# Performance work log

Measured on AMD Instinct MI355X. Metric: run time of the kernel, lower is better.

The kernel has to match this reference:

```python
import jax, jax.numpy as jnp
import numpy as np

B, T, E, H = 2, 2048, 1024, 16


def setup_inputs() -> dict:
    key = jax.random.key(0)
    ks = jax.random.split(key, 6)
    s = lambda k, shape: jax.random.normal(k, shape, dtype=jnp.float32) * 0.02
    return {
        "x": jax.random.normal(ks[0], (B, T, E), dtype=jnp.float32),
        "ln1_g": jnp.ones((E,), jnp.float32),
        "ln1_b": jnp.zeros((E,), jnp.float32),
        "attn_w": s(ks[1], (E, 3 * E)),
        "attn_b": jnp.zeros((3 * E,), jnp.float32),
        "proj_w": s(ks[2], (E, E)),
        "proj_b": jnp.zeros((E,), jnp.float32),
        "ln2_g": jnp.ones((E,), jnp.float32),
        "ln2_b": jnp.zeros((E,), jnp.float32),
        "mlp_w1": s(ks[3], (E, 4 * E)),
        "mlp_b1": jnp.zeros((4 * E,), jnp.float32),
        "mlp_w2": s(ks[4], (4 * E, E)),
        "mlp_b2": jnp.zeros((E,), jnp.float32),
        "w_att": jnp.ones((1,), jnp.float32),
        "w_mlp": jnp.ones((1,), jnp.float32),
    }


def _ln(x, g, b, eps=1e-5):
    m = x.mean(-1, keepdims=True)
    v = ((x - m) ** 2).mean(-1, keepdims=True)
    return (x - m) * jax.lax.rsqrt(v + eps) * g + b


def reference(x, ln1_g, ln1_b, attn_w, attn_b, proj_w, proj_b,
              ln2_g, ln2_b, mlp_w1, mlp_b1, mlp_w2, mlp_b2, w_att, w_mlp):
    Bx, Tx, Ex = x.shape
    hd = Ex // H
    # --- self-attention on ln_1(x) ---
    qkv = _ln(x, ln1_g, ln1_b) @ attn_w + attn_b          # [B,T,3E]
    q, k, v = jnp.split(qkv, 3, axis=-1)
    q = q.reshape(Bx, Tx, H, hd)
    k = k.reshape(Bx, Tx, H, hd)
    v = v.reshape(Bx, Tx, H, hd)
    att = jnp.einsum('bthd,bshd->bhts', q, k) * (1.0 / np.sqrt(hd))  # [B,H,T,T]
    causal = jnp.tril(jnp.ones((Tx, Tx), dtype=bool))
    att = jnp.where(causal, att, -jnp.inf)
    att = jax.nn.softmax(att, axis=-1)
    y = jnp.einsum('bhts,bshd->bthd', att, v).reshape(Bx, Tx, Ex)
    y = y @ proj_w + proj_b
    x = x * w_att + y
    # --- MLP on ln_2(x) ---
    h = _ln(x, ln2_g, ln2_b) @ mlp_w1 + mlp_b1
    h = jax.nn.gelu(h, approximate=False)
    x = x * w_mlp + (h @ mlp_w2 + mlp_b2)
    return x
```

## Files before the change

kernel.cpp:

```cpp
#include <hip/hip_runtime.h>
#include <math.h>

typedef __bf16 bf16;
typedef bf16 bf16x8 __attribute__((ext_vector_type(8)));
typedef bf16 bf16x4 __attribute__((ext_vector_type(4)));
typedef float f32x4 __attribute__((ext_vector_type(4)));

#define MFMA(a, b, c) __builtin_amdgcn_mfma_f32_16x16x32_bf16((a), (b), (c), 0, 0, 0)

#define GLOAD_LDS16(gp, lp)                                                        \
  __builtin_amdgcn_global_load_lds((const __attribute__((address_space(1))) void*)(gp), \
                                   (__attribute__((address_space(3))) void*)(lp), 16, 0, 0)

static const size_t E_WT_ATTN = 0;
static const size_t E_WT_PROJ = 3145728;
static const size_t E_WT_MLP1 = 4194304;
static const size_t E_WT_MLP2 = 8388608;
static const size_t E_LN1     = 12582912;
static const size_t E_QKV     = 16777216;
static const size_t E_VT      = 37748736;
static const size_t E_Y       = 41943040;
static const size_t E_LN2     = 46137344;
static const size_t E_H       = 50331648;
static const size_t BYTE_X2    = 134217728;
static const size_t BYTE_OPART = 150994944;
static const size_t BYTE_ML    = 184549376;
static const size_t BYTE_GPART = 185597952;
static const size_t TOTAL_BYTES = 252706816;

__device__ __align__(4096) unsigned char g_buf[TOTAL_BYTES];

__global__ __launch_bounds__(256) void transpose_all(const float* __restrict__ aw,
                                                     const float* __restrict__ pw,
                                                     const float* __restrict__ m1,
                                                     const float* __restrict__ m2,
                                                     bf16* __restrict__ o_a,
                                                     bf16* __restrict__ o_p,
                                                     bf16* __restrict__ o_m1,
                                                     bf16* __restrict__ o_m2) {
  __shared__ float tile[32][33];
  int bid = blockIdx.x;
  const float* in;
  bf16* out;
  int K, N, tix;
  if (bid < 3072) { in = aw; out = o_a; K = 1024; N = 3072; tix = bid; }
  else if (bid < 4096) { in = pw; out = o_p; K = 1024; N = 1024; tix = bid - 3072; }
  else if (bid < 8192) { in = m1; out = o_m1; K = 1024; N = 4096; tix = bid - 4096; }
  else { in = m2; out = o_m2; K = 4096; N = 1024; tix = bid - 8192; }
  int ntx = N >> 5;
  int bx = tix % ntx, by = tix / ntx;
  int tx = threadIdx.x, ty = threadIdx.y;
#pragma unroll
  for (int i = ty; i < 32; i += 8)
    tile[i][tx] = in[(size_t)(by * 32 + i) * N + bx * 32 + tx];
  __syncthreads();
#pragma unroll
  for (int i = ty; i < 32; i += 8)
    out[(size_t)(bx * 32 + i) * K + by * 32 + tx] = (bf16)tile[tx][i];
}

__global__ __launch_bounds__(256) void ln_bf16(const float* __restrict__ x,
                                               const float* __restrict__ g,
                                               const float* __restrict__ b,
                                               bf16* __restrict__ out) {
  int row = blockIdx.x, tid = threadIdx.x;
  const float* xr = x + ((size_t)row << 10);
  float4 v = *(const float4*)(xr + tid * 4);
  float s = v.x + v.y + v.z + v.w;
  float ss = v.x * v.x + v.y * v.y + v.z * v.z + v.w * v.w;
#pragma unroll
  for (int off = 32; off >= 1; off >>= 1) {
    s += __shfl_down(s, off);
    ss += __shfl_down(ss, off);
  }
  __shared__ float sh[8];
  int wid = tid >> 6;
  if ((tid & 63) == 0) { sh[wid] = s; sh[wid + 4] = ss; }
  __syncthreads();
  float ts = sh[0] + sh[1] + sh[2] + sh[3];
  float tss = sh[4] + sh[5] + sh[6] + sh[7];
  float mean = ts * (1.0f / 1024.0f);
  float var = tss * (1.0f / 1024.0f) - mean * mean;
  float inv = rsqrtf(var + 1e-5f);
  float4 gg = *(const float4*)(g + tid * 4);
  float4 bb = *(const float4*)(b + tid * 4);
  bf16x4 o;
  o[0] = (bf16)((v.x - mean) * inv * gg.x + bb.x);
  o[1] = (bf16)((v.y - mean) * inv * gg.y + bb.y);
  o[2] = (bf16)((v.z - mean) * inv * gg.z + bb.z);
  o[3] = (bf16)((v.w - mean) * inv * gg.w + bb.w);
  *(bf16x4*)(out + ((size_t)row << 10) + tid * 4) = o;
}

template <int EPI>
__global__ __launch_bounds__(512, 2) void gemm256(const bf16* __restrict__ A,
                                                  const bf16* __restrict__ Bt,
                                                  const float* __restrict__ bias,
                                                  bf16* __restrict__ outb,
                                                  float* __restrict__ outf,
                                                  int M, int N, int K, int Kseg) {
  __shared__ __align__(16) bf16 As[2][16384];
  __shared__ __align__(16) bf16 Bs[2][16384];
  int tid = threadIdx.x;
  int nwg = gridDim.x * gridDim.y;
  int bid = blockIdx.y * gridDim.x + blockIdx.x;
  int id2 = ((nwg & 7) == 0) ? ((bid & 7) * (nwg >> 3) + (bid >> 3)) : bid;
  int bx = id2 % gridDim.x, by = id2 / gridDim.x;
  int lane = tid & 63, wid = tid >> 6;
  int wr = wid >> 2, wc = wid & 3;
  int g = lane >> 4, lr = lane & 15;
  f32x4 acc[8][4];
#pragma unroll
  for (int m = 0; m < 8; ++m)
#pragma unroll
    for (int n = 0; n < 4; ++n) acc[m][n] = (f32x4){0.f, 0.f, 0.f, 0.f};
  const bf16* Ab = A + (size_t)by * 256 * K;
  const bf16* Bb = Bt + (size_t)bx * 256 * K;
  int rbase = tid >> 3;
  int srccol = (((tid & 7) ^ (rbase & 7)) << 3);
  const bf16* Asrc = Ab + (size_t)rbase * K + srccol;
  const bf16* Bsrc = Bb + (size_t)rbase * K + srccol;
#define G256_STAGE(buf, k0)                                                \
  {                                                                        \
    _Pragma("unroll") for (int q = 0; q < 4; ++q) {                        \
      GLOAD_LDS16(Asrc + (size_t)(q * 64) * K + (k0), &As[buf][tid * 8 + q * 4096]); \
      GLOAD_LDS16(Bsrc + (size_t)(q * 64) * K + (k0), &Bs[buf][tid * 8 + q * 4096]); \
    }                                                                      \
  }
  int kbeg = blockIdx.z * Kseg;
  int NT = Kseg >> 6;
  G256_STAGE(0, kbeg);
  if (NT > 1) {
    G256_STAGE(1, kbeg + 64);
    asm volatile("s_waitcnt vmcnt(8)" ::: "memory");
  } else {
    asm volatile("s_waitcnt vmcnt(0)" ::: "memory");
  }
  __builtin_amdgcn_sched_barrier(0);
  __builtin_amdgcn_s_barrier();
  int c = 0;
  for (int t = 0; t < NT; ++t) {
    bf16x8 a0[8], b0[4], a1[8], b1[4];
#pragma unroll
    for (int m = 0; m < 8; ++m) {
      int row = wr * 128 + m * 16 + lr;
      a0[m] = *(const bf16x8*)&As[c][row * 64 + ((g ^ (row & 7)) << 3)];
      a1[m] = *(const bf16x8*)&As[c][row * 64 + (((4 + g) ^ (row & 7)) << 3)];
    }
#pragma unroll
    for (int n = 0; n < 4; ++n) {
      int row = wc * 64 + n * 16 + lr;
      b0[n] = *(const bf16x8*)&Bs[c][row * 64 + ((g ^ (row & 7)) << 3)];
      b1[n] = *(const bf16x8*)&Bs[c][row * 64 + (((4 + g) ^ (row & 7)) << 3)];
    }
#pragma unroll
    for (int m = 0; m < 8; ++m)
#pragma unroll
      for (int n = 0; n < 4; ++n) acc[m][n] = MFMA(a0[m], b0[n], acc[m][n]);
    asm volatile("s_waitcnt lgkmcnt(0)" ::: "memory");
    __builtin_amdgcn_sched_barrier(0);
    __builtin_amdgcn_s_barrier();
    if (t + 2 < NT) G256_STAGE(c, kbeg + (t + 2) * 64);
#pragma unroll
    for (int m = 0; m < 8; ++m)
#pragma unroll
      for (int n = 0; n < 4; ++n) acc[m][n] = MFMA(a1[m], b1[n], acc[m][n]);
    if (t + 2 < NT) {
      asm volatile("s_waitcnt vmcnt(8)" ::: "memory");
    } else if (t + 1 < NT) {
      asm volatile("s_waitcnt vmcnt(0)" ::: "memory");
    }
    __builtin_amdgcn_sched_barrier(0);
    __builtin_amdgcn_s_barrier();
    c ^= 1;
  }
#undef G256_STAGE
  if (EPI == 3) {
    float* po = outf + (size_t)blockIdx.z * M * N;
#pragma unroll
    for (int m = 0; m < 8; ++m) {
#pragma unroll
      for (int n = 0; n < 4; ++n) {
        int rg0 = by * 256 + wr * 128 + m * 16 + g * 4;
        int cg = bx * 256 + wc * 64 + n * 16 + lr;
#pragma unroll
        for (int j = 0; j < 4; ++j) po[(size_t)(rg0 + j) * N + cg] = acc[m][n][j];
      }
    }
  } else {
#pragma unroll
    for (int m = 0; m < 8; ++m) {
#pragma unroll
      for (int n = 0; n < 4; ++n) {
        int rg0 = by * 256 + wr * 128 + m * 16 + g * 4;
        int cg = bx * 256 + wc * 64 + n * 16 + lr;
        float bv = bias[cg];
#pragma unroll
        for (int j = 0; j < 4; ++j) {
          float v = acc[m][n][j] + bv;
          size_t idx = (size_t)(rg0 + j) * N + cg;
          if (EPI == 0)
            outb[idx] = (bf16)v;
          else {
            float u = 0.7978845608f * (v + 0.044715f * v * v * v);
            float e = exp2f(u * 2.885390082f);
            float th = 1.0f - 2.0f / (e + 1.0f);
            outb[idx] = (bf16)(0.5f * v * (1.0f + th));
          }
        }
      }
    }
  }
}

__global__ __launch_bounds__(256) void gemm_bt3(const bf16* __restrict__ A,
                                                const bf16* __restrict__ Bt,
                                                float* __restrict__ outf,
                                                int M, int N, int K, int Kseg) {
  __shared__ __align__(16) bf16 As[128 * 32];
  __shared__ __align__(16) bf16 Bs[128 * 32];
  int bx = blockIdx.x, by = blockIdx.y;
  int tid = threadIdx.x;
  int lane = tid & 63, wid = tid >> 6;
  int wr = wid >> 1, wc = wid & 1;
  int g = lane >> 4, lr = lane & 15;
  f32x4 acc[4][4];
#pragma unroll
  for (int m = 0; m < 4; ++m)
#pragma unroll
    for (int n = 0; n < 4; ++n) acc[m][n] = (f32x4){0.f, 0.f, 0.f, 0.f};
  const bf16* Ab = A + (size_t)by * 128 * K;
  const bf16* Bb = Bt + (size_t)bx * 128 * K;
  int srow = tid >> 2;
  int sk8 = (tid & 3) * 8;
  const bf16* Ap0 = Ab + (size_t)srow * K + sk8;
  const bf16* Ap1 = Ab + (size_t)(srow + 64) * K + sk8;
  const bf16* Bp0 = Bb + (size_t)srow * K + sk8;
  const bf16* Bp1 = Bb + (size_t)(srow + 64) * K + sk8;
  bf16* lA0 = As + tid * 8;
  bf16* lA1 = As + 2048 + tid * 8;
  bf16* lB0 = Bs + tid * 8;
  bf16* lB1 = Bs + 2048 + tid * 8;
  int kbeg = blockIdx.z * Kseg;
  int kend = kbeg + Kseg;
  for (int k0 = kbeg; k0 < kend; k0 += 32) {
    GLOAD_LDS16(Ap0 + k0, lA0);
    GLOAD_LDS16(Ap1 + k0, lA1);
    GLOAD_LDS16(Bp0 + k0, lB0);
    GLOAD_LDS16(Bp1 + k0, lB1);
    __syncthreads();
    bf16x8 af[4], bfv[4];
#pragma unroll
    for (int m = 0; m < 4; ++m) af[m] = *(const bf16x8*)(As + (wr * 64 + m * 16 + lr) * 32 + g * 8);
#pragma unroll
    for (int n = 0; n < 4; ++n) bfv[n] = *(const bf16x8*)(Bs + (wc * 64 + n * 16 + lr) * 32 + g * 8);
#pragma unroll
    for (int m = 0; m < 4; ++m)
#pragma unroll
      for (int n = 0; n < 4; ++n) acc[m][n] = MFMA(af[m], bfv[n], acc[m][n]);
    __syncthreads();
  }
  float* po = outf + (size_t)blockIdx.z * M * N;
#pragma unroll
  for (int m = 0; m < 4; ++m) {
#pragma unroll
    for (int n = 0; n < 4; ++n) {
      int rg0 = by * 128 + wr * 64 + m * 16 + g * 4;
      int cg = bx * 128 + wc * 64 + n * 16 + lr;
#pragma unroll
      for (int j = 0; j < 4; ++j) po[(size_t)(rg0 + j) * N + cg] = acc[m][n][j];
    }
  }
}

template <int SK>
__global__ __launch_bounds__(256) void reduce_add(const float* __restrict__ part,
                                                  const float* __restrict__ bias,
                                                  const float* __restrict__ res,
                                                  const float* __restrict__ wsc,
                                                  float* __restrict__ out, int MN, int N) {
  size_t i = ((size_t)blockIdx.x * 256 + threadIdx.x) * 4;
  float4 a = *(const float4*)(part + i);
#pragma unroll
  for (int s = 1; s < SK; ++s) {
    float4 b = *(const float4*)(part + (size_t)s * MN + i);
    a.x += b.x; a.y += b.y; a.z += b.z; a.w += b.w;
  }
  int col = (int)(i & (size_t)(N - 1));
  float4 bv = *(const float4*)(bias + col);
  float4 rv = *(const float4*)(res + i);
  float w = wsc[0];
  float4 o;
  o.x = rv.x * w + a.x + bv.x;
  o.y = rv.y * w + a.y + bv.y;
  o.z = rv.z * w + a.z + bv.z;
  o.w = rv.w * w + a.w + bv.w;
  *(float4*)(out + i) = o;
}

__global__ __launch_bounds__(256) void reduce_ln(const float* __restrict__ part,
                                                 const float* __restrict__ bias,
                                                 const float* __restrict__ res,
                                                 const float* __restrict__ wsc,
                                                 const float* __restrict__ lng,
                                                 const float* __restrict__ lnb,
                                                 float* __restrict__ x2out,
                                                 bf16* __restrict__ lnout) {
  int row = blockIdx.x, tid = threadIdx.x;
  size_t i = ((size_t)row << 10) + tid * 4;
  float4 a = *(const float4*)(part + i);
  float4 b2 = *(const float4*)(part + 4194304 + i);
  float4 rv = *(const float4*)(res + i);
  float4 bv = *(const float4*)(bias + tid * 4);
  float w = wsc[0];
  float4 o;
  o.x = rv.x * w + a.x + b2.x + bv.x;
  o.y = rv.y * w + a.y + b2.y + bv.y;
  o.z = rv.z * w + a.z + b2.z + bv.z;
  o.w = rv.w * w + a.w + b2.w + bv.w;
  *(float4*)(x2out + i) = o;
  float s = o.x + o.y + o.z + o.w;
  float ss = o.x * o.x + o.y * o.y + o.z * o.z + o.w * o.w;
#pragma unroll
  for (int off = 32; off >= 1; off >>= 1) {
    s += __shfl_down(s, off);
    ss += __shfl_down(ss, off);
  }
  __shared__ float sh[8];
  int wid = tid >> 6;
  if ((tid & 63) == 0) { sh[wid] = s; sh[wid + 4] = ss; }
  __syncthreads();
  float ts = sh[0] + sh[1] + sh[2] + sh[3];
  float tss = sh[4] + sh[5] + sh[6] + sh[7];
  float mean = ts * (1.0f / 1024.0f);
  float var = tss * (1.0f / 1024.0f) - mean * mean;
  float inv = rsqrtf(var + 1e-5f);
  float4 gg = *(const float4*)(lng + tid * 4);
  float4 bb = *(const float4*)(lnb + tid * 4);
  bf16x4 ov;
  ov[0] = (bf16)((o.x - mean) * inv * gg.x + bb.x);
  ov[1] = (bf16)((o.y - mean) * inv * gg.y + bb.y);
  ov[2] = (bf16)((o.z - mean) * inv * gg.z + bb.z);
  ov[3] = (bf16)((o.w - mean) * inv * gg.w + bb.w);
  *(bf16x4*)(lnout + ((size_t)row << 10) + tid * 4) = ov;
}

__global__ __launch_bounds__(256) void split_v_t(const bf16* __restrict__ qkv,
                                                 bf16* __restrict__ vT) {
  int t0 = blockIdx.x * 32;
  int bh = blockIdx.y;
  int b = bh >> 4, h = bh & 15;
  __shared__ bf16 tile[32][72];
  int tid = threadIdx.x;
  int d = tid & 63, tl0 = tid >> 6;
#pragma unroll
  for (int p = 0; p < 8; ++p) {
    int tl = p * 4 + tl0;
    tile[tl][d] = qkv[((size_t)(b * 2048 + t0 + tl)) * 3072 + 2048 + h * 64 + d];
  }
  __syncthreads();
  int tl = tid & 31, dq = tid >> 5;
#pragma unroll
  for (int p = 0; p < 8; ++p) {
    int dd = p * 8 + dq;
    vT[((size_t)(bh * 64 + dd)) * 2048 + t0 + tl] = tile[tl][dd];
  }
}

__global__ __launch_bounds__(256) void attn_fwd(const bf16* __restrict__ qkv,
                                                const bf16* __restrict__ vT,
                                                float* __restrict__ o_part,
                                                float* __restrict__ ml_part) {
  __shared__ __align__(16) bf16 Ks[2][4096];
  __shared__ __align__(16) bf16 Vs[2][4096];
  __shared__ bf16 P[4][16][72];
  int id = blockIdx.x;
  int bh = id & 31;
  int seg = (id >> 5) & 1;
  int qi = ((id >> 6) + bh) & 31;
  int tid = threadIdx.x, wid = tid >> 6, lane = tid & 63;
  int g = lane >> 4, lr = lane & 15;
  int b = bh >> 4, h = bh & 15;
  int nk = qi + 1;
  int n0 = (nk + 1) >> 1;
  int kt0 = seg ? n0 : 0;
  int kt1 = seg ? nk : n0;
  int qrow = qi * 64 + wid * 16 + lr;
  const bf16* Qr = qkv + ((size_t)(b * 2048 + qrow)) * 3072 + h * 64;
  const float beta = 0.18033688f;
  bf16x8 qf[2];
  qf[0] = *(const bf16x8*)(Qr + g * 8);
  qf[1] = *(const bf16x8*)(Qr + 32 + g * 8);
#pragma unroll
  for (int kk = 0; kk < 2; ++kk)
#pragma unroll
    for (int e = 0; e < 8; ++e) qf[kk][e] = (bf16)((float)qf[kk][e] * beta);
  int r0 = tid >> 3, cs0 = ((tid & 7) ^ (r0 & 7)) << 3;
  int c1i = tid + 256;
  int r1 = c1i >> 3, cs1 = ((c1i & 7) ^ (r1 & 7)) << 3;
  const bf16* sK0 = qkv + ((size_t)(b * 2048 + r0)) * 3072 + 1024 + h * 64 + cs0;
  const bf16* sK1 = qkv + ((size_t)(b * 2048 + r1)) * 3072 + 1024 + h * 64 + cs1;
  const bf16* sV0 = vT + (size_t)bh * 131072 + (size_t)r0 * 2048 + cs0;
  const bf16* sV1 = vT + (size_t)bh * 131072 + (size_t)r1 * 2048 + cs1;
  bf16* dK0 = &Ks[0][0] + tid * 8;
  bf16* dK1 = &Ks[0][0] + 2048 + tid * 8;
  bf16* dV0 = &Vs[0][0] + tid * 8;
  bf16* dV1 = &Vs[0][0] + 2048 + tid * 8;
#define ATTN_STAGE(bufsel, ktv)                          \
  {                                                      \
    size_t kadv = (size_t)(ktv) * (64 * 3072);           \
    size_t vadv = (size_t)(ktv) * 64;                    \
    int bo = (bufsel) * 4096;                            \
    GLOAD_LDS16(sK0 + kadv, dK0 + bo);                   \
    GLOAD_LDS16(sK1 + kadv, dK1 + bo);                   \
    GLOAD_LDS16(sV0 + vadv, dV0 + bo);                   \
    GLOAD_LDS16(sV1 + vadv, dV1 + bo);                   \
  }
  f32x4 o[4];
#pragma unroll
  for (int n = 0; n < 4; ++n) o[n] = (f32x4){0.f, 0.f, 0.f, 0.f};
  float m = -3e38f, l = 0.f;
  if (kt0 < kt1) ATTN_STAGE(0, kt0);
  __syncthreads();
  int sw = lr & 7;
  int sb = (lane & 48) | (g << 2);
  for (int kt = kt0; kt < kt1; ++kt) {
    int cur = (kt - kt0) & 1;
    if (kt + 1 < kt1) ATTN_STAGE(cur ^ 1, kt + 1);
    const bf16* Kb = &Ks[cur][0];
    const bf16* Vb = &Vs[cur][0];
    f32x4 s[4];
#pragma unroll
    for (int n = 0; n < 4; ++n) s[n] = (f32x4){0.f, 0.f, 0.f, 0.f};
#pragma unroll
    for (int kk = 0; kk < 2; ++kk) {
#pragma unroll
      for (int n = 0; n < 4; ++n) {
        bf16x8 kf = *(const bf16x8*)(Kb + ((n * 16 + lr) << 6) + ((((kk << 2) + g) ^ sw) << 3));
        s[n] = MFMA(kf, qf[kk], s[n]);
      }
    }
    if (kt == qi) {
      int kc0 = kt * 64 + g * 4;
#pragma unroll
      for (int n = 0; n < 4; ++n)
#pragma unroll
        for (int j = 0; j < 4; ++j)
          if ((kc0 + n * 16 + j) > qrow) s[n][j] = -3e38f;
    }
    float mx = s[0][0];
#pragma unroll
    for (int n = 0; n < 4; ++n)
#pragma unroll
      for (int j = 0; j < 4; ++j) mx = fmaxf(mx, s[n][j]);
    mx = fmaxf(mx, __shfl_xor(mx, 16));
    mx = fmaxf(mx, __shfl_xor(mx, 32));
    bool defer = __all(mx <= m + 11.5416f);
    float mn = m, al = 0.f;
    if (!defer) {
      mn = fmaxf(m, mx);
      al = exp2f(m - mn);
      m = mn;
    }
    float rs = 0.f;
    bf16x4 pw[4];
#pragma unroll
    for (int n = 0; n < 4; ++n)
#pragma unroll
      for (int j = 0; j < 4; ++j) {
        float p = exp2f(s[n][j] - mn);
        rs += p;
        pw[n][j] = (bf16)p;
      }
    rs += __shfl_xor(rs, 16);
    rs += __shfl_xor(rs, 32);
    if (defer) {
      l += rs;
    } else {
      l = l * al + rs;
      float alj[4];
#pragma unroll
      for (int j = 0; j < 4; ++j) alj[j] = __shfl(al, sb + j);
#pragma unroll
      for (int n = 0; n < 4; ++n)
#pragma unroll
        for (int j = 0; j < 4; ++j) o[n][j] *= alj[j];
    }
#pragma unroll
    for (int n = 0; n < 4; ++n) *(bf16x4*)&P[wid][lr][n * 16 + g * 4] = pw[n];
#pragma unroll
    for (int kk = 0; kk < 2; ++kk) {
      bf16x8 pf = *(const bf16x8*)&P[wid][lr][kk * 32 + g * 8];
#pragma unroll
      for (int n = 0; n < 4; ++n) {
        bf16x8 vf = *(const bf16x8*)(Vb + ((n * 16 + lr) << 6) + ((((kk << 2) + g) ^ sw) << 3));
        o[n] = MFMA(pf, vf, o[n]);
      }
    }
    __syncthreads();
  }
  float* ob = o_part + (size_t)id * 4096;
#pragma unroll
  for (int n = 0; n < 4; ++n)
#pragma unroll
    for (int j = 0; j < 4; ++j)
      ob[(size_t)(wid * 16 + g * 4 + j) * 64 + n * 16 + lr] = o[n][j];
  if (lane < 16) {
    ml_part[(size_t)id * 128 + (wid * 16 + lane) * 2] = m;
    ml_part[(size_t)id * 128 + (wid * 16 + lane) * 2 + 1] = l;
  }
#undef ATTN_STAGE
}

__global__ __launch_bounds__(256) void attn_combine(const float* __restrict__ o_part,
                                                    const float* __restrict__ ml_part,
                                                    bf16* __restrict__ y) {
  int c = blockIdx.x;
  int bh = c & 31, qi = c >> 5;
  int b = bh >> 4, h = bh & 15;
  int qraw = (qi - bh) & 31;
  size_t id0 = (size_t)bh + ((size_t)qraw << 6);
  size_t id1 = id0 + 32;
  int t = threadIdx.x;
  int r = t >> 2, cq = (t & 3) << 4;
  float m1 = ml_part[id0 * 128 + r * 2], l1 = ml_part[id0 * 128 + r * 2 + 1];
  float m2 = ml_part[id1 * 128 + r * 2], l2 = ml_part[id1 * 128 + r * 2 + 1];
  float mm = fmaxf(m1, m2);
  float w1 = exp2f(m1 - mm), w2 = exp2f(m2 - mm);
  float inv = 1.0f / (l1 * w1 + l2 * w2);
  const float* p1 = o_part + id0 * 4096 + r * 64 + cq;
  const float* p2 = o_part + id1 * 4096 + r * 64 + cq;
  bf16* yp = y + ((size_t)(b * 2048 + qi * 64 + r)) * 1024 + h * 64 + cq;
#pragma unroll
  for (int u = 0; u < 4; ++u) {
    float4 a = *(const float4*)(p1 + u * 4);
    float4 bq = *(const float4*)(p2 + u * 4);
    bf16x4 ov;
    ov[0] = (bf16)((a.x * w1 + bq.x * w2) * inv);
    ov[1] = (bf16)((a.y * w1 + bq.y * w2) * inv);
    ov[2] = (bf16)((a.z * w1 + bq.z * w2) * inv);
    ov[3] = (bf16)((a.w * w1 + bq.w * w2) * inv);
    *(bf16x4*)(yp + u * 4) = ov;
  }
}

extern "C" void kernel_launch(void* const* d_in, const int* in_sizes, int n_in,
                              void* d_out, int out_size, void* d_ws, size_t ws_size,
                              hipStream_t stream) {
  const float* x = (const float*)d_in[0];
  const float* ln1_g = (const float*)d_in[1];
  const float* ln1_b = (const float*)d_in[2];
  const float* attn_w = (const float*)d_in[3];
  const float* attn_b = (const float*)d_in[4];
  const float* proj_w = (const float*)d_in[5];
  const float* proj_b = (const float*)d_in[6];
  const float* ln2_g = (const float*)d_in[7];
  const float* ln2_b = (const float*)d_in[8];
  const float* mlp_w1 = (const float*)d_in[9];
  const float* mlp_b1 = (const float*)d_in[10];
  const float* mlp_w2 = (const float*)d_in[11];
  const float* mlp_b2 = (const float*)d_in[12];
  const float* w_att = (const float*)d_in[13];
  const float* w_mlp = (const float*)d_in[14];
  float* out = (float*)d_out;

  unsigned char* base = nullptr;
  if (ws_size >= TOTAL_BYTES) {
    base = (unsigned char*)d_ws;
  } else {
    hipGetSymbolAddress((void**)&base, HIP_SYMBOL(g_buf));
  }
  bf16* bb = (bf16*)base;
  bf16* wt_attn = bb + E_WT_ATTN;
  bf16* wt_proj = bb + E_WT_PROJ;
  bf16* wt_mlp1 = bb + E_WT_MLP1;
  bf16* wt_mlp2 = bb + E_WT_MLP2;
  bf16* ln1o = bb + E_LN1;
  bf16* qkv = bb + E_QKV;
  bf16* vTb = bb + E_VT;
  bf16* yb = bb + E_Y;
  bf16* ln2o = bb + E_LN2;
  bf16* hb = bb + E_H;
  float* x2 = (float*)(base + BYTE_X2);
  float* o_part = (float*)(base + BYTE_OPART);
  float* ml_part = (float*)(base + BYTE_ML);
  float* gpart = (float*)(base + BYTE_GPART);

  transpose_all<<<12288, dim3(32, 8), 0, stream>>>(attn_w, proj_w, mlp_w1, mlp_w2,
                                                   wt_attn, wt_proj, wt_mlp1, wt_mlp2);

  ln_bf16<<<4096, 256, 0, stream>>>(x, ln1_g, ln1_b, ln1o);

  gemm256<0><<<dim3(12, 16, 1), 512, 0, stream>>>(ln1o, wt_attn, attn_b, qkv, nullptr,
                                                  4096, 3072, 1024, 1024);

  split_v_t<<<dim3(64, 32), 256, 0, stream>>>(qkv, vTb);

  attn_fwd<<<2048, 256, 0, stream>>>(qkv, vTb, o_part, ml_part);
  attn_combine<<<1024, 256, 0, stream>>>(o_part, ml_part, yb);

  gemm_bt3<<<dim3(8, 32, 2), 256, 0, stream>>>(yb, wt_proj, gpart, 4096, 1024, 1024, 512);
  reduce_ln<<<4096, 256, 0, stream>>>(gpart, proj_b, x, w_att, ln2_g, ln2_b, x2, ln2o);

  gemm256<1><<<dim3(16, 16, 1), 512, 0, stream>>>(ln2o, wt_mlp1, mlp_b1, hb, nullptr,
                                                  4096, 4096, 1024, 1024);

  gemm256<3><<<dim3(4, 16, 4), 512, 0, stream>>>(hb, wt_mlp2, nullptr, nullptr, gpart,
                                                 4096, 1024, 4096, 1024);
  reduce_add<4><<<4096, 256, 0, stream>>>(gpart, mlp_b2, x2, w_mlp, out, 4194304, 1024);
}
```

Baseline: 373.9 us.

## Process two KV tiles per attention iteration with split K/V prefetch and setprio

```diff
diff --git a/kernel.cpp b/kernel.cpp
--- a/kernel.cpp
+++ b/kernel.cpp
@@ -153,18 +153,22 @@
       b0[n] = *(const bf16x8*)&Bs[c][row * 64 + ((g ^ (row & 7)) << 3)];
       b1[n] = *(const bf16x8*)&Bs[c][row * 64 + (((4 + g) ^ (row & 7)) << 3)];
     }
+    __builtin_amdgcn_s_setprio(1);
 #pragma unroll
     for (int m = 0; m < 8; ++m)
 #pragma unroll
       for (int n = 0; n < 4; ++n) acc[m][n] = MFMA(a0[m], b0[n], acc[m][n]);
+    __builtin_amdgcn_s_setprio(0);
     asm volatile("s_waitcnt lgkmcnt(0)" ::: "memory");
     __builtin_amdgcn_sched_barrier(0);
     __builtin_amdgcn_s_barrier();
     if (t + 2 < NT) G256_STAGE(c, kbeg + (t + 2) * 64);
+    __builtin_amdgcn_s_setprio(1);
 #pragma unroll
     for (int m = 0; m < 8; ++m)
 #pragma unroll
       for (int n = 0; n < 4; ++n) acc[m][n] = MFMA(a1[m], b1[n], acc[m][n]);
+    __builtin_amdgcn_s_setprio(0);
     if (t + 2 < NT) {
       asm volatile("s_waitcnt vmcnt(8)" ::: "memory");
     } else if (t + 1 < NT) {
@@ -373,7 +377,7 @@
                                                 float* __restrict__ ml_part) {
   __shared__ __align__(16) bf16 Ks[2][4096];
   __shared__ __align__(16) bf16 Vs[2][4096];
-  __shared__ bf16 P[4][16][72];
+  __shared__ bf16 P[4][16][136];
   int id = blockIdx.x;
   int bh = id & 31;
   int seg = (id >> 5) & 1;
@@ -385,6 +389,7 @@
   int n0 = (nk + 1) >> 1;
   int kt0 = seg ? n0 : 0;
   int kt1 = seg ? nk : n0;
+  int nt = kt1 - kt0;
   int qrow = qi * 64 + wid * 16 + lr;
   const bf16* Qr = qkv + ((size_t)(b * 2048 + qrow)) * 3072 + h * 64;
   const float beta = 0.18033688f;
@@ -406,53 +411,71 @@
   bf16* dK1 = &Ks[0][0] + 2048 + tid * 8;
   bf16* dV0 = &Vs[0][0] + tid * 8;
   bf16* dV1 = &Vs[0][0] + 2048 + tid * 8;
-#define ATTN_STAGE(bufsel, ktv)                          \
-  {                                                      \
-    size_t kadv = (size_t)(ktv) * (64 * 3072);           \
-    size_t vadv = (size_t)(ktv) * 64;                    \
-    int bo = (bufsel) * 4096;                            \
-    GLOAD_LDS16(sK0 + kadv, dK0 + bo);                   \
-    GLOAD_LDS16(sK1 + kadv, dK1 + bo);                   \
-    GLOAD_LDS16(sV0 + vadv, dV0 + bo);                   \
-    GLOAD_LDS16(sV1 + vadv, dV1 + bo);                   \
+#define STAGE_K(bufsel, ktv)                              \
+  {                                                       \
+    size_t kadv = (size_t)(ktv) * (64 * 3072);            \
+    int bo = (bufsel) * 4096;                             \
+    GLOAD_LDS16(sK0 + kadv, dK0 + bo);                    \
+    GLOAD_LDS16(sK1 + kadv, dK1 + bo);                    \
+  }
+#define STAGE_V(bufsel, ktv)                              \
+  {                                                       \
+    size_t vadv = (size_t)(ktv) * 64;                     \
+    int bo = (bufsel) * 4096;                             \
+    GLOAD_LDS16(sV0 + vadv, dV0 + bo);                    \
+    GLOAD_LDS16(sV1 + vadv, dV1 + bo);                    \
   }
   f32x4 o[4];
 #pragma unroll
   for (int n = 0; n < 4; ++n) o[n] = (f32x4){0.f, 0.f, 0.f, 0.f};
   float m = -3e38f, l = 0.f;
-  if (kt0 < kt1) ATTN_STAGE(0, kt0);
-  __syncthreads();
   int sw = lr & 7;
   int sb = (lane & 48) | (g << 2);
-  for (int kt = kt0; kt < kt1; ++kt) {
-    int cur = (kt - kt0) & 1;
-    if (kt + 1 < kt1) ATTN_STAGE(cur ^ 1, kt + 1);
-    const bf16* Kb = &Ks[cur][0];
-    const bf16* Vb = &Vs[cur][0];
-    f32x4 s[4];
-#pragma unroll
-    for (int n = 0; n < 4; ++n) s[n] = (f32x4){0.f, 0.f, 0.f, 0.f};
+  if (nt > 0) {
+    STAGE_K(0, kt0);
+    STAGE_K(1, kt0 + 1);
+    STAGE_V(0, kt0);
+    STAGE_V(1, kt0 + 1);
+  }
+  int kt = kt0;
+  for (; kt + 2 <= kt1; kt += 2) {
+    asm volatile("s_waitcnt vmcnt(4)" ::: "memory");
+    __builtin_amdgcn_sched_barrier(0);
+    __builtin_amdgcn_s_barrier();
+    f32x4 s0[4], s1[4];
+#pragma unroll
+    for (int n = 0; n < 4; ++n) { s0[n] = (f32x4){0.f,0.f,0.f,0.f}; s1[n] = (f32x4){0.f,0.f,0.f,0.f}; }
+    __builtin_amdgcn_s_setprio(1);
 #pragma unroll
     for (int kk = 0; kk < 2; ++kk) {
 #pragma unroll
       for (int n = 0; n < 4; ++n) {
-        bf16x8 kf = *(const bf16x8*)(Kb + ((n * 16 + lr) << 6) + ((((kk << 2) + g) ^ sw) << 3));
-        s[n] = MFMA(kf, qf[kk], s[n]);
+        int off = ((n * 16 + lr) << 6) + ((((kk << 2) + g) ^ sw) << 3);
+        bf16x8 kf0 = *(const bf16x8*)(&Ks[0][0] + off);
+        s0[n] = MFMA(kf0, qf[kk], s0[n]);
+        bf16x8 kf1 = *(const bf16x8*)(&Ks[1][0] + off);
+        s1[n] = MFMA(kf1, qf[kk], s1[n]);
       }
     }
-    if (kt == qi) {
-      int kc0 = kt * 64 + g * 4;
+    __builtin_amdgcn_s_setprio(0);
+    asm volatile("s_waitcnt lgkmcnt(0)" ::: "memory");
+    __builtin_amdgcn_sched_barrier(0);
+    __builtin_amdgcn_s_barrier();
+    STAGE_K(0, kt + 2);
+    STAGE_K(1, kt + 3);
+    if (kt + 1 == qi) {
+      int kc0 = (kt + 1) * 64 + g * 4;
 #pragma unroll
       for (int n = 0; n < 4; ++n)
 #pragma unroll
         for (int j = 0; j < 4; ++j)
-          if ((kc0 + n * 16 + j) > qrow) s[n][j] = -3e38f;
-    }
-    float mx = s[0][0];
+          if ((kc0 + n * 16 + j) > qrow) s1[n][j] = -3e38f;
+    }
+    float mx = s0[0][0];
 #pragma unroll
     for (int n = 0; n < 4; ++n)
 #pragma unroll
-      for (int j = 0; j < 4; ++j) mx = fmaxf(mx, s[n][j]);
+      for (int j = 0; j < 4; ++j) { mx = fmaxf(mx, s0[n][j]); mx = fmaxf(mx, s1[n][j]); }
     mx = fmaxf(mx, __shfl_xor(mx, 16));
     mx = fmaxf(mx, __shfl_xor(mx, 32));
     bool defer = __all(mx <= m + 11.5416f);
@@ -463,14 +486,16 @@
       m = mn;
     }
     float rs = 0.f;
-    bf16x4 pw[4];
+    bf16x4 pw0[4], pw1[4];
 #pragma unroll
     for (int n = 0; n < 4; ++n)
 #pragma unroll
       for (int j = 0; j < 4; ++j) {
-        float p = exp2f(s[n][j] - mn);
-        rs += p;
-        pw[n][j] = (bf16)p;
+        float p0 = exp2f(s0[n][j] - mn);
+        float p1 = exp2f(s1[n][j] - mn);
+        rs += p0 + p1;
+        pw0[n][j] = (bf16)p0;
+        pw1[n][j] = (bf16)p1;
       }
     rs += __shfl_xor(rs, 16);
     rs += __shfl_xor(rs, 32);
@@ -487,17 +512,116 @@
         for (int j = 0; j < 4; ++j) o[n][j] *= alj[j];
     }
 #pragma unroll
-    for (int n = 0; n < 4; ++n) *(bf16x4*)&P[wid][lr][n * 16 + g * 4] = pw[n];
+    for (int n = 0; n < 4; ++n) {
+      *(bf16x4*)&P[wid][lr][n * 16 + g * 4] = pw0[n];
+      *(bf16x4*)&P[wid][lr][64 + n * 16 + g * 4] = pw1[n];
+    }
+    asm volatile("s_waitcnt vmcnt(4)" ::: "memory");
+    __builtin_amdgcn_sched_barrier(0);
+    __builtin_amdgcn_s_barrier();
+    __builtin_amdgcn_s_setprio(1);
+#pragma unroll
+    for (int kk = 0; kk < 2; ++kk) {
+      bf16x8 pf0 = *(const bf16x8*)&P[wid][lr][kk * 32 + g * 8];
+      bf16x8 pf1 = *(const bf16x8*)&P[wid][lr][64 + kk * 32 + g * 8];
+#pragma unroll
+      for (int n = 0; n < 4; ++n) {
+        int off = ((n * 16 + lr) << 6) + ((((kk << 2) + g) ^ sw) << 3);
+        bf16x8 vf0 = *(const bf16x8*)(&Vs[0][0] + off);
+        o[n] = MFMA(pf0, vf0, o[n]);
+        bf16x8 vf1 = *(const bf16x8*)(&Vs[1][0] + off);
+        o[n] = MFMA(pf1, vf1, o[n]);
+      }
+    }
+    __builtin_amdgcn_s_setprio(0);
+    asm volatile("s_waitcnt lgkmcnt(0)" ::: "memory");
+    __builtin_amdgcn_sched_barrier(0);
+    __builtin_amdgcn_s_barrier();
+    STAGE_V(0, kt + 2);
+    STAGE_V(1, kt + 3);
+  }
+  if (kt < kt1) {
+    int lb = (kt - kt0) & 1;
+    asm volatile("s_waitcnt vmcnt(4)" ::: "memory");
+    __builtin_amdgcn_sched_barrier(0);
+    __builtin_amdgcn_s_barrier();
+    f32x4 s0[4];
+#pragma unroll
+    for (int n = 0; n < 4; ++n) s0[n] = (f32x4){0.f,0.f,0.f,0.f};
+    __builtin_amdgcn_s_setprio(1);
+#pragma unroll
+    for (int kk = 0; kk < 2; ++kk) {
+#pragma unroll
+      for (int n = 0; n < 4; ++n) {
+        int off = ((n * 16 + lr) << 6) + ((((kk << 2) + g) ^ sw) << 3);
+        bf16x8 kf = *(const bf16x8*)(&Ks[lb][0] + off);
+        s0[n] = MFMA(kf, qf[kk], s0[n]);
+      }
+    }
+    __builtin_amdgcn_s_setprio(0);
+    if (kt == qi) {
+      int kc0 = kt * 64 + g * 4;
+#pragma unroll
+      for (int n = 0; n < 4; ++n)
+#pragma unroll
+        for (int j = 0; j < 4; ++j)
+          if ((kc0 + n * 16 + j) > qrow) s0[n][j] = -3e38f;
+    }
+    float mx = s0[0][0];
+#pragma unroll
+    for (int n = 0; n < 4; ++n)
+#pragma unroll
+      for (int j = 0; j < 4; ++j) mx = fmaxf(mx, s0[n][j]);
+    mx = fmaxf(mx, __shfl_xor(mx, 16));
+    mx = fmaxf(mx, __shfl_xor(mx, 32));
+    bool defer = __all(mx <= m + 11.5416f);
+    float mn = m, al = 0.f;
+    if (!defer) {
+      mn = fmaxf(m, mx);
+      al = exp2f(m - mn);
+      m = mn;
+    }
+    float rs = 0.f;
+    bf16x4 pw0[4];
+#pragma unroll
+    for (int n = 0; n < 4; ++n)
+#pragma unroll
+      for (int j = 0; j < 4; ++j) {
+        float p = exp2f(s0[n][j] - mn);
+        rs += p;
+        pw0[n][j] = (bf16)p;
+      }
+    rs += __shfl_xor(rs, 16);
+    rs += __shfl_xor(rs, 32);
+    if (defer) {
+      l += rs;
+    } else {
+      l = l * al + rs;
+      float alj[4];
+#pragma unroll
+      for (int j = 0; j < 4; ++j) alj[j] = __shfl(al, sb + j);
+#pragma unroll
+      for (int n = 0; n < 4; ++n)
+#pragma unroll
+        for (int j = 0; j < 4; ++j) o[n][j] *= alj[j];
+    }
+#pragma unroll
+    for (int n = 0; n < 4; ++n) *(bf16x4*)&P[wid][lr][n * 16 + g * 4] = pw0[n];
+    asm volatile("s_waitcnt vmcnt(0)" ::: "memory");
+    __builtin_amdgcn_sched_barrier(0);
+    __builtin_amdgcn_s_barrier();
+    __builtin_amdgcn_s_setprio(1);
 #pragma unroll
     for (int kk = 0; kk < 2; ++kk) {
       bf16x8 pf = *(const bf16x8*)&P[wid][lr][kk * 32 + g * 8];
 #pragma unroll
       for (int n = 0; n < 4; ++n) {
-        bf16x8 vf = *(const bf16x8*)(Vb + ((n * 16 + lr) << 6) + ((((kk << 2) + g) ^ sw) << 3));
+        int off = ((n * 16 + lr) << 6) + ((((kk << 2) + g) ^ sw) << 3);
+        bf16x8 vf = *(const bf16x8*)(&Vs[lb][0] + off);
         o[n] = MFMA(pf, vf, o[n]);
       }
     }
-    __syncthreads();
+    __builtin_amdgcn_s_setprio(0);
   }
   float* ob = o_part + (size_t)id * 4096;
 #pragma unroll
@@ -509,7 +633,8 @@
     ml_part[(size_t)id * 128 + (wid * 16 + lane) * 2] = m;
     ml_part[(size_t)id * 128 + (wid * 16 + lane) * 2 + 1] = l;
   }
-#undef ATTN_STAGE
+#undef STAGE_K
+#undef STAGE_V
 }
 
 __global__ __launch_bounds__(256) void attn_combine(const float* __restrict__ o_part,
```

After: 369.3 us. No clear change (-1.2%).
